# Kernel optimization log

Measured on AMD Instinct MI355X. Metric: run time of the kernel, lower is better.

The kernel has to match this reference:

```python
import jax, jax.numpy as jnp
import numpy as np

NEG_BIG = -1.0e9


def setup_inputs() -> dict:
    key = jax.random.key(0)
    ks = jax.random.split(key, 6)
    B, H, L, D = 2, 16, 2048, 64
    q = jax.random.normal(ks[0], (B, H, L, D), dtype=jnp.float32)
    k = jax.random.normal(ks[1], (B, H, L, D), dtype=jnp.float32)
    v = jax.random.normal(ks[2], (B, H, L, D), dtype=jnp.float32)
    p_q = jax.random.normal(ks[3], (B, L, 3), dtype=jnp.float32)
    p_k = jax.random.normal(ks[4], (B, L, 3), dtype=jnp.float32)
    mask = jax.random.randint(ks[5], (B, L), 0, 2, dtype=jnp.int32)
    return {"q": q, "k": k, "v": v, "p_q": p_q, "p_k": p_k, "mask": mask}


def reference(q, k, v, p_q, p_k, mask):
    # learned score function instantiated as scaled dot-product: [B,H,Lq,Lk]
    d_head = q.shape[-1]
    scores = jnp.einsum("bhqd,bhkd->bhqk", q, k) / jnp.sqrt(jnp.float32(d_head))
    # mask: [B, Lk] -> [B, 1, 1, Lk]; additive -1e9 on masked keys
    m = mask.astype(scores.dtype)[:, None, None, :]
    scores = scores + m * NEG_BIG
    # softplus normalization (instead of softmax), scaled by key length v.shape[2]
    Lk = v.shape[2]
    scores = jax.nn.softplus(scores) / Lk
    out = jnp.einsum("bhqk,bhkd->bhqd", scores, v)
    return (out, scores)
```

## Files before the change

kernel.cpp:

```cpp
#include <hip/hip_runtime.h>

typedef float f32x4  __attribute__((ext_vector_type(4)));
typedef float f32x16 __attribute__((ext_vector_type(16)));
typedef short s16x8  __attribute__((ext_vector_type(8)));
typedef unsigned int u32;
typedef unsigned int u32x4 __attribute__((ext_vector_type(4)));
typedef unsigned short u16;

#define LL 2048
#define DD 64
#define NITER 32
#define SC_OFF 4194304ull

struct SMem {
    u16 Khi[2][64][72];
    u16 VT [2][64][72];
    unsigned char P[4][4096];
};

__device__ __forceinline__ u32 cvt_pk_bf16(float lo, float hi) {
    u32 r;
    asm("v_cvt_pk_bf16_f32 %0, %1, %2" : "=v"(r) : "v"(lo), "v"(hi));
    return r;
}

__global__ __launch_bounds__(512, 4)
void psam_kernel(const float* __restrict__ Qg0, const float* __restrict__ Kg0,
                 const float* __restrict__ Vg0, const int* __restrict__ Mg0,
                 float* __restrict__ out)
{
    __shared__ SMem sm;
    const int tid = threadIdx.x;
    const int w = tid >> 6, l = tid & 63;
    const int j31 = l & 31, h = l >> 5;
    const int cw = w & 1, iw = w >> 1;
    const int cwj = cw * 32 + j31;

    const int bid = ((int)blockIdx.x & 7) * 64 + ((int)blockIdx.x >> 3);
    const int bh = bid >> 4;
    const int m0 = (bid & 15) << 7;
    const int bB = bh >> 4;

    const float* Kg = Kg0 + (size_t)bh * LL * DD;
    const float* Vg = Vg0 + (size_t)bh * LL * DD;
    const int*   Mg = Mg0 + (size_t)bB * LL;
    float* So = out + SC_OFF + (size_t)bh * LL * LL + (size_t)m0 * LL;
    float* Oo = out + ((size_t)bh * LL + m0) * DD;

    s16x8 qf[4];
    {
        const float* qr = Qg0 + ((size_t)bh * LL + m0 + iw * 32 + j31) * DD + h * 8;
#pragma unroll
        for (int ks = 0; ks < 4; ++ks) {
            f32x4 a = *(const f32x4*)(qr + ks * 16);
            f32x4 b = *(const f32x4*)(qr + ks * 16 + 4);
            u32x4 qp;
            qp[0] = cvt_pk_bf16(a[0], a[1]);
            qp[1] = cvt_pk_bf16(a[2], a[3]);
            qp[2] = cvt_pk_bf16(b[0], b[1]);
            qp[3] = cvt_pk_bf16(b[2], b[3]);
            qf[ks] = __builtin_bit_cast(s16x8, qp);
        }
    }

    const int kc = tid >> 3, kd = (tid & 7) * 8;
    const int vc = tid & 63, vd = (tid >> 6) * 8;
    f32x4 kvx, kvy, vvx, vvy;
    {
        const f32x4* s = (const f32x4*)(Kg + (size_t)kc * DD + kd);
        f32x4 x = s[0], y = s[1];
        u32x4 kp;
        kp[0] = cvt_pk_bf16(x[0], x[1]);
        kp[1] = cvt_pk_bf16(x[2], x[3]);
        kp[2] = cvt_pk_bf16(y[0], y[1]);
        kp[3] = cvt_pk_bf16(y[2], y[3]);
        *(u32x4*)&sm.Khi[0][kc][kd] = kp;
        const f32x4* s2 = (const f32x4*)(Vg + (size_t)vc * DD + vd);
        f32x4 vx = s2[0], vy = s2[1];
#pragma unroll
        for (int i = 0; i < 2; ++i) {
            u32 a0 = cvt_pk_bf16(vx[2 * i], vx[2 * i + 1]);
            sm.VT[0][vd + 2 * i][vc]     = (u16)a0;
            sm.VT[0][vd + 2 * i + 1][vc] = (u16)(a0 >> 16);
            u32 a1 = cvt_pk_bf16(vy[2 * i], vy[2 * i + 1]);
            sm.VT[0][vd + 4 + 2 * i][vc]     = (u16)a1;
            sm.VT[0][vd + 4 + 2 * i + 1][vc] = (u16)(a1 >> 16);
        }
    }
    {
        const f32x4* s = (const f32x4*)(Kg + (size_t)(64 + kc) * DD + kd);
        kvx = s[0]; kvy = s[1];
        const f32x4* s2 = (const f32x4*)(Vg + (size_t)(64 + vc) * DD + vd);
        vvx = s2[0]; vvy = s2[1];
    }
    float blc = -1.0e9f * (float)Mg[cwj];
    float bln = -1.0e9f * (float)Mg[64 + cwj];

    f32x16 accO;
#pragma unroll
    for (int e = 0; e < 16; ++e) accO[e] = 0.0f;

    unsigned char* spw = &sm.P[iw][0];
    asm volatile("s_waitcnt lgkmcnt(0)" ::: "memory");
    __builtin_amdgcn_s_barrier();

    f32x16 pA;
#pragma unroll
    for (int e = 0; e < 16; ++e) pA[e] = 0.0f;
    float* spA = So;

    int buf = 0;
    for (int t = 0; t < NITER; ++t) {
        f32x16 accS;
#pragma unroll
        for (int e = 0; e < 16; ++e) accS[e] = 0.0f;
#pragma unroll
        for (int ks = 0; ks < 4; ++ks) {
            s16x8 kf = *(const s16x8*)&sm.Khi[buf][cwj][ks * 16 + h * 8];
            accS = __builtin_amdgcn_mfma_f32_32x32x16_bf16(qf[ks], kf, accS, 0, 0, 0);
        }
        const float bl = blc;
        float* sp = So + (size_t)(iw * 32 + 4 * h) * LL + t * 64 + cwj;
        f32x16 pc;
#pragma unroll
        for (int g = 0; g < 4; ++g) {
#pragma unroll
            for (int r = 0; r < 4; ++r) {
                float x  = accS[g * 4 + r] * 0.125f + bl;
                float tt = __builtin_amdgcn_exp2f(x * 1.44269504f);
                float p  = __builtin_amdgcn_logf(1.0f + tt) * 3.38450771757785852e-4f;
                pc[g * 4 + r] = p;
                const int il = 8 * g + 4 * h + r;
                *(u16*)(spw + ((il * 128 + cwj * 2) ^ ((il & 7) << 4))) = (u16)cvt_pk_bf16(p, p);
            }
        }
        if ((t & 1) == 0) {
            pA = pc; spA = sp;
        } else {
#pragma unroll
            for (int g = 0; g < 4; ++g)
#pragma unroll
                for (int r = 0; r < 4; ++r) {
                    float* ra = spA + (size_t)(8 * g + r) * LL;
                    __builtin_nontemporal_store(pA[g * 4 + r], ra);
                    __builtin_nontemporal_store(pc[g * 4 + r], ra + 64);
                }
        }
        asm volatile("s_waitcnt lgkmcnt(0)" ::: "memory");
        __builtin_amdgcn_s_barrier();

#pragma unroll
        for (int ks = 0; ks < 4; ++ks) {
            s16x8 va = *(const s16x8*)&sm.VT[buf][cwj][ks * 16 + h * 8];
            s16x8 pb = *(const s16x8*)(spw + ((j31 * 128 + ks * 32 + h * 16) ^ ((j31 & 7) << 4)));
            accO = __builtin_amdgcn_mfma_f32_32x32x16_bf16(va, pb, accO, 0, 0, 0);
        }

        if (t + 1 < NITER) {
            u32x4 kp;
            kp[0] = cvt_pk_bf16(kvx[0], kvx[1]);
            kp[1] = cvt_pk_bf16(kvx[2], kvx[3]);
            kp[2] = cvt_pk_bf16(kvy[0], kvy[1]);
            kp[3] = cvt_pk_bf16(kvy[2], kvy[3]);
            *(u32x4*)&sm.Khi[buf ^ 1][kc][kd] = kp;
#pragma unroll
            for (int i = 0; i < 2; ++i) {
                u32 a0 = cvt_pk_bf16(vvx[2 * i], vvx[2 * i + 1]);
                sm.VT[buf ^ 1][vd + 2 * i][vc]     = (u16)a0;
                sm.VT[buf ^ 1][vd + 2 * i + 1][vc] = (u16)(a0 >> 16);
                u32 a1 = cvt_pk_bf16(vvy[2 * i], vvy[2 * i + 1]);
                sm.VT[buf ^ 1][vd + 4 + 2 * i][vc]     = (u16)a1;
                sm.VT[buf ^ 1][vd + 4 + 2 * i + 1][vc] = (u16)(a1 >> 16);
            }
        }
        {
            const int tp = (t + 2 < NITER) ? (t + 2) : (NITER - 1);
            const f32x4* s1 = (const f32x4*)(Kg + (size_t)(tp * 64 + kc) * DD + kd);
            kvx = s1[0]; kvy = s1[1];
            const f32x4* s2 = (const f32x4*)(Vg + (size_t)(tp * 64 + vc) * DD + vd);
            vvx = s2[0]; vvy = s2[1];
            blc = bln;
            bln = -1.0e9f * (float)Mg[tp * 64 + cwj];
        }
        asm volatile("s_waitcnt lgkmcnt(0)" ::: "memory");
        __builtin_amdgcn_s_barrier();
        buf ^= 1;
    }

#pragma unroll
    for (int g = 0; g < 4; ++g) {
        f32x4 o;
#pragma unroll
        for (int r = 0; r < 4; ++r) o[r] = accO[g * 4 + r];
        *(f32x4*)(Oo + (size_t)(iw * 32 + j31) * DD + cw * 32 + h * 4 + g * 8) = o;
    }
}

extern "C" void kernel_launch(void* const* d_in, const int* in_sizes, int n_in,
                              void* d_out, int out_size, void* d_ws, size_t ws_size,
                              hipStream_t stream) {
    const float* q    = (const float*)d_in[0];
    const float* k    = (const float*)d_in[1];
    const float* v    = (const float*)d_in[2];
    const int*   mask = (const int*)d_in[5];
    float* out = (float*)d_out;
    hipLaunchKernelGGL(psam_kernel, dim3(512), dim3(512), 0, stream, q, k, v, mask, out);
}
```

Baseline: 122.3 us.

## Make P tile wave-private and split PV by key half to drop a barrier

Each wave now writes its own 32x32 bf16 probability tile into a private LDS slot and multiplies it against both halves of V^T over only its own 32 keys. That removes the cross-wave dependency on P, so the workgroup barrier between the score and PV phases is dropped. Each wave therefore produces a partial O covering all 64 head dimensions, and the partial O values from the two key-half waves are summed through LDS once after the loop. The cost is a second accumulator (more VGPRs) and an extra LDS reduction plus barrier at the end.

```diff
diff --git a/kernel.cpp b/kernel.cpp
--- a/kernel.cpp
+++ b/kernel.cpp
@@ -15,7 +15,7 @@
 struct SMem {
     u16 Khi[2][64][72];
     u16 VT [2][64][72];
-    unsigned char P[4][4096];
+    u16 P[8][32][40];
 };
 
 __device__ __forceinline__ u32 cvt_pk_bf16(float lo, float hi) {
@@ -96,11 +96,11 @@
     float blc = -1.0e9f * (float)Mg[cwj];
     float bln = -1.0e9f * (float)Mg[64 + cwj];
 
-    f32x16 accO;
-#pragma unroll
-    for (int e = 0; e < 16; ++e) accO[e] = 0.0f;
-
-    unsigned char* spw = &sm.P[iw][0];
+    f32x16 accO0, accO1;
+#pragma unroll
+    for (int e = 0; e < 16; ++e) { accO0[e] = 0.0f; accO1[e] = 0.0f; }
+
+    u16* spw = &sm.P[w][0][0];
     asm volatile("s_waitcnt lgkmcnt(0)" ::: "memory");
     __builtin_amdgcn_s_barrier();
 
@@ -131,7 +131,7 @@
                 float p  = __builtin_amdgcn_logf(1.0f + tt) * 3.38450771757785852e-4f;
                 pc[g * 4 + r] = p;
                 const int il = 8 * g + 4 * h + r;
-                *(u16*)(spw + ((il * 128 + cwj * 2) ^ ((il & 7) << 4))) = (u16)cvt_pk_bf16(p, p);
+                spw[il * 40 + j31] = (u16)cvt_pk_bf16(p, p);
             }
         }
         if ((t & 1) == 0) {
@@ -147,13 +147,14 @@
                 }
         }
         asm volatile("s_waitcnt lgkmcnt(0)" ::: "memory");
-        __builtin_amdgcn_s_barrier();
-
-#pragma unroll
-        for (int ks = 0; ks < 4; ++ks) {
-            s16x8 va = *(const s16x8*)&sm.VT[buf][cwj][ks * 16 + h * 8];
-            s16x8 pb = *(const s16x8*)(spw + ((j31 * 128 + ks * 32 + h * 16) ^ ((j31 & 7) << 4)));
-            accO = __builtin_amdgcn_mfma_f32_32x32x16_bf16(va, pb, accO, 0, 0, 0);
+
+#pragma unroll
+        for (int ks2 = 0; ks2 < 2; ++ks2) {
+            s16x8 pb = *(const s16x8*)(spw + j31 * 40 + ks2 * 16 + h * 8);
+            s16x8 va0 = *(const s16x8*)&sm.VT[buf][j31][cw * 32 + ks2 * 16 + h * 8];
+            accO0 = __builtin_amdgcn_mfma_f32_32x32x16_bf16(va0, pb, accO0, 0, 0, 0);
+            s16x8 va1 = *(const s16x8*)&sm.VT[buf][32 + j31][cw * 32 + ks2 * 16 + h * 8];
+            accO1 = __builtin_amdgcn_mfma_f32_32x32x16_bf16(va1, pb, accO1, 0, 0, 0);
         }
 
         if (t + 1 < NITER) {
@@ -187,12 +188,38 @@
         buf ^= 1;
     }
 
-#pragma unroll
-    for (int g = 0; g < 4; ++g) {
-        f32x4 o;
-#pragma unroll
-        for (int r = 0; r < 4; ++r) o[r] = accO[g * 4 + r];
-        *(f32x4*)(Oo + (size_t)(iw * 32 + j31) * DD + cw * 32 + h * 4 + g * 8) = o;
+    float* red = (float*)&sm;
+    if (cw == 1) {
+#pragma unroll
+        for (int db = 0; db < 2; ++db) {
+            const f32x16& a = db ? accO1 : accO0;
+#pragma unroll
+            for (int g = 0; g < 4; ++g)
+#pragma unroll
+                for (int r = 0; r < 4; ++r) {
+                    const int row = db * 32 + 8 * g + 4 * h + r;
+                    red[(size_t)(iw * 64 + row) * 32 + j31] = a[g * 4 + r];
+                }
+        }
+    }
+    asm volatile("s_waitcnt lgkmcnt(0)" ::: "memory");
+    __builtin_amdgcn_s_barrier();
+    if (cw == 0) {
+        float* op = Oo + (size_t)(iw * 32 + j31) * DD;
+#pragma unroll
+        for (int db = 0; db < 2; ++db) {
+            const f32x16& a = db ? accO1 : accO0;
+#pragma unroll
+            for (int g = 0; g < 4; ++g) {
+                f32x4 o;
+#pragma unroll
+                for (int r = 0; r < 4; ++r) {
+                    const int row = db * 32 + 8 * g + 4 * h + r;
+                    o[r] = a[g * 4 + r] + red[(size_t)(iw * 64 + row) * 32 + j31];
+                }
+                *(f32x4*)(op + db * 32 + 8 * g + 4 * h) = o;
+            }
+        }
     }
 }
 
```

After: 121.4 us (median of 2 runs). About the same (-0.7%).

## Give each wave full 64-key strips and double the query tile per block

Applied to the files above, without the earlier changes.

Each block now covers 256 query rows, with each of the 8 waves owning 32 rows and all 64 keys per step, so the grid shrinks from 512 to 256 blocks. Every K/V tile loaded into LDS is now reused across twice as many queries. Each wave keeps its own padded P buffer, which removes the barrier between the softplus write and the PV MFMA. Score stores are batched across four iterations to write 256-float contiguous runs. The cost is higher register pressure (launch bounds lowered to 2 blocks per SM, six extra 16-float accumulators) and fewer blocks to spread across the CUs.

```diff
diff --git a/kernel.cpp b/kernel.cpp
--- a/kernel.cpp
+++ b/kernel.cpp
@@ -15,7 +15,7 @@
 struct SMem {
     u16 Khi[2][64][72];
     u16 VT [2][64][72];
-    unsigned char P[4][4096];
+    u16 P  [8][32][72];
 };
 
 __device__ __forceinline__ u32 cvt_pk_bf16(float lo, float hi) {
@@ -24,7 +24,7 @@
     return r;
 }
 
-__global__ __launch_bounds__(512, 4)
+__global__ __launch_bounds__(512, 2)
 void psam_kernel(const float* __restrict__ Qg0, const float* __restrict__ Kg0,
                  const float* __restrict__ Vg0, const int* __restrict__ Mg0,
                  float* __restrict__ out)
@@ -33,12 +33,10 @@
     const int tid = threadIdx.x;
     const int w = tid >> 6, l = tid & 63;
     const int j31 = l & 31, h = l >> 5;
-    const int cw = w & 1, iw = w >> 1;
-    const int cwj = cw * 32 + j31;
-
-    const int bid = ((int)blockIdx.x & 7) * 64 + ((int)blockIdx.x >> 3);
-    const int bh = bid >> 4;
-    const int m0 = (bid & 15) << 7;
+
+    const int bid = ((int)blockIdx.x & 7) * 32 + ((int)blockIdx.x >> 3);
+    const int bh = bid >> 3;
+    const int m0 = (bid & 7) << 8;
     const int bB = bh >> 4;
 
     const float* Kg = Kg0 + (size_t)bh * LL * DD;
@@ -49,7 +47,7 @@
 
     s16x8 qf[4];
     {
-        const float* qr = Qg0 + ((size_t)bh * LL + m0 + iw * 32 + j31) * DD + h * 8;
+        const float* qr = Qg0 + ((size_t)bh * LL + m0 + w * 32 + j31) * DD + h * 8;
 #pragma unroll
         for (int ks = 0; ks < 4; ++ks) {
             f32x4 a = *(const f32x4*)(qr + ks * 16);
@@ -93,106 +91,131 @@
         const f32x4* s2 = (const f32x4*)(Vg + (size_t)(64 + vc) * DD + vd);
         vvx = s2[0]; vvy = s2[1];
     }
-    float blc = -1.0e9f * (float)Mg[cwj];
-    float bln = -1.0e9f * (float)Mg[64 + cwj];
-
-    f32x16 accO;
-#pragma unroll
-    for (int e = 0; e < 16; ++e) accO[e] = 0.0f;
-
-    unsigned char* spw = &sm.P[iw][0];
+    float blo = -1.0e9f * (float)Mg[j31];
+    float bhi = -1.0e9f * (float)Mg[32 + j31];
+    float nlo = -1.0e9f * (float)Mg[64 + j31];
+    float nhi = -1.0e9f * (float)Mg[96 + j31];
+
+    f32x16 accO0, accO1;
+#pragma unroll
+    for (int e = 0; e < 16; ++e) { accO0[e] = 0.0f; accO1[e] = 0.0f; }
+
+    u16* spw = &sm.P[w][0][0];
     asm volatile("s_waitcnt lgkmcnt(0)" ::: "memory");
     __builtin_amdgcn_s_barrier();
 
-    f32x16 pA;
-#pragma unroll
-    for (int e = 0; e < 16; ++e) pA[e] = 0.0f;
-    float* spA = So;
-
-    int buf = 0;
-    for (int t = 0; t < NITER; ++t) {
-        f32x16 accS;
-#pragma unroll
-        for (int e = 0; e < 16; ++e) accS[e] = 0.0f;
-#pragma unroll
-        for (int ks = 0; ks < 4; ++ks) {
-            s16x8 kf = *(const s16x8*)&sm.Khi[buf][cwj][ks * 16 + h * 8];
-            accS = __builtin_amdgcn_mfma_f32_32x32x16_bf16(qf[ks], kf, accS, 0, 0, 0);
-        }
-        const float bl = blc;
-        float* sp = So + (size_t)(iw * 32 + 4 * h) * LL + t * 64 + cwj;
-        f32x16 pc;
+    f32x16 dAlo, dAhi, dBlo, dBhi, dClo, dChi;
+
+    for (int t4 = 0; t4 < NITER / 4; ++t4) {
+#pragma unroll
+        for (int p = 0; p < 4; ++p) {
+            const int t = t4 * 4 + p;
+            const int buf = p & 1;
+
+            f32x16 aS0, aS1;
+#pragma unroll
+            for (int e = 0; e < 16; ++e) { aS0[e] = 0.0f; aS1[e] = 0.0f; }
+#pragma unroll
+            for (int ks = 0; ks < 4; ++ks) {
+                s16x8 kf0 = *(const s16x8*)&sm.Khi[buf][j31][ks * 16 + h * 8];
+                aS0 = __builtin_amdgcn_mfma_f32_32x32x16_bf16(qf[ks], kf0, aS0, 0, 0, 0);
+                s16x8 kf1 = *(const s16x8*)&sm.Khi[buf][32 + j31][ks * 16 + h * 8];
+                aS1 = __builtin_amdgcn_mfma_f32_32x32x16_bf16(qf[ks], kf1, aS1, 0, 0, 0);
+            }
+
+            f32x16 plo, phi;
+#pragma unroll
+            for (int g = 0; g < 4; ++g) {
+#pragma unroll
+                for (int r = 0; r < 4; ++r) {
+                    const int e = g * 4 + r;
+                    float x0  = aS0[e] * 0.125f + blo;
+                    float t0  = __builtin_amdgcn_exp2f(x0 * 1.44269504f);
+                    plo[e] = __builtin_amdgcn_logf(1.0f + t0) * 3.38450771757785852e-4f;
+                    float x1  = aS1[e] * 0.125f + bhi;
+                    float t1  = __builtin_amdgcn_exp2f(x1 * 1.44269504f);
+                    phi[e] = __builtin_amdgcn_logf(1.0f + t1) * 3.38450771757785852e-4f;
+                    const int il = 8 * g + 4 * h + r;
+                    spw[il * 72 + j31]      = (u16)cvt_pk_bf16(plo[e], plo[e]);
+                    spw[il * 72 + 32 + j31] = (u16)cvt_pk_bf16(phi[e], phi[e]);
+                }
+            }
+
+            if (p == 0)      { dAlo = plo; dAhi = phi; }
+            else if (p == 1) { dBlo = plo; dBhi = phi; }
+            else if (p == 2) { dClo = plo; dChi = phi; }
+            else {
+                float* base = So + (size_t)(w * 32 + 4 * h) * LL + (size_t)(t4 * 4) * 64 + j31;
+#pragma unroll
+                for (int g = 0; g < 4; ++g)
+#pragma unroll
+                    for (int r = 0; r < 4; ++r) {
+                        const int e = g * 4 + r;
+                        float* ra = base + (size_t)(8 * g + r) * LL;
+                        __builtin_nontemporal_store(dAlo[e], ra);
+                        __builtin_nontemporal_store(dAhi[e], ra + 32);
+                        __builtin_nontemporal_store(dBlo[e], ra + 64);
+                        __builtin_nontemporal_store(dBhi[e], ra + 96);
+                        __builtin_nontemporal_store(dClo[e], ra + 128);
+                        __builtin_nontemporal_store(dChi[e], ra + 160);
+                        __builtin_nontemporal_store(plo[e],  ra + 192);
+                        __builtin_nontemporal_store(phi[e],  ra + 224);
+                    }
+            }
+            asm volatile("s_waitcnt lgkmcnt(0)" ::: "memory");
+
+#pragma unroll
+            for (int ks2 = 0; ks2 < 4; ++ks2) {
+                s16x8 pb = *(const s16x8*)((const char*)spw + j31 * 144 + ks2 * 32 + h * 16);
+                s16x8 va0 = *(const s16x8*)&sm.VT[buf][j31][ks2 * 16 + h * 8];
+                accO0 = __builtin_amdgcn_mfma_f32_32x32x16_bf16(va0, pb, accO0, 0, 0, 0);
+                s16x8 va1 = *(const s16x8*)&sm.VT[buf][32 + j31][ks2 * 16 + h * 8];
+                accO1 = __builtin_amdgcn_mfma_f32_32x32x16_bf16(va1, pb, accO1, 0, 0, 0);
+            }
+
+            if (t + 1 < NITER) {
+                u32x4 kp;
+                kp[0] = cvt_pk_bf16(kvx[0], kvx[1]);
+                kp[1] = cvt_pk_bf16(kvx[2], kvx[3]);
+                kp[2] = cvt_pk_bf16(kvy[0], kvy[1]);
+                kp[3] = cvt_pk_bf16(kvy[2], kvy[3]);
+                *(u32x4*)&sm.Khi[buf ^ 1][kc][kd] = kp;
+#pragma unroll
+                for (int i = 0; i < 2; ++i) {
+                    u32 a0 = cvt_pk_bf16(vvx[2 * i], vvx[2 * i + 1]);
+                    sm.VT[buf ^ 1][vd + 2 * i][vc]     = (u16)a0;
+                    sm.VT[buf ^ 1][vd + 2 * i + 1][vc] = (u16)(a0 >> 16);
+                    u32 a1 = cvt_pk_bf16(vvy[2 * i], vvy[2 * i + 1]);
+                    sm.VT[buf ^ 1][vd + 4 + 2 * i][vc]     = (u16)a1;
+                    sm.VT[buf ^ 1][vd + 4 + 2 * i + 1][vc] = (u16)(a1 >> 16);
+                }
+            }
+            {
+                const int tp = (t + 2 < NITER) ? (t + 2) : (NITER - 1);
+                const f32x4* s1 = (const f32x4*)(Kg + (size_t)(tp * 64 + kc) * DD + kd);
+                kvx = s1[0]; kvy = s1[1];
+                const f32x4* s2 = (const f32x4*)(Vg + (size_t)(tp * 64 + vc) * DD + vd);
+                vvx = s2[0]; vvy = s2[1];
+                blo = nlo; bhi = nhi;
+                nlo = -1.0e9f * (float)Mg[tp * 64 + j31];
+                nhi = -1.0e9f * (float)Mg[tp * 64 + 32 + j31];
+            }
+            asm volatile("s_waitcnt lgkmcnt(0)" ::: "memory");
+            __builtin_amdgcn_s_barrier();
+        }
+    }
+
+    float* op = Oo + (size_t)(w * 32 + j31) * DD;
+#pragma unroll
+    for (int db = 0; db < 2; ++db) {
+        const f32x16& a = db ? accO1 : accO0;
 #pragma unroll
         for (int g = 0; g < 4; ++g) {
-#pragma unroll
-            for (int r = 0; r < 4; ++r) {
-                float x  = accS[g * 4 + r] * 0.125f + bl;
-                float tt = __builtin_amdgcn_exp2f(x * 1.44269504f);
-                float p  = __builtin_amdgcn_logf(1.0f + tt) * 3.38450771757785852e-4f;
-                pc[g * 4 + r] = p;
-                const int il = 8 * g + 4 * h + r;
-                *(u16*)(spw + ((il * 128 + cwj * 2) ^ ((il & 7) << 4))) = (u16)cvt_pk_bf16(p, p);
-            }
-        }
-        if ((t & 1) == 0) {
-            pA = pc; spA = sp;
-        } else {
-#pragma unroll
-            for (int g = 0; g < 4; ++g)
-#pragma unroll
-                for (int r = 0; r < 4; ++r) {
-                    float* ra = spA + (size_t)(8 * g + r) * LL;
-                    __builtin_nontemporal_store(pA[g * 4 + r], ra);
-                    __builtin_nontemporal_store(pc[g * 4 + r], ra + 64);
-                }
-        }
-        asm volatile("s_waitcnt lgkmcnt(0)" ::: "memory");
-        __builtin_amdgcn_s_barrier();
-
-#pragma unroll
-        for (int ks = 0; ks < 4; ++ks) {
-            s16x8 va = *(const s16x8*)&sm.VT[buf][cwj][ks * 16 + h * 8];
-            s16x8 pb = *(const s16x8*)(spw + ((j31 * 128 + ks * 32 + h * 16) ^ ((j31 & 7) << 4)));
-            accO = __builtin_amdgcn_mfma_f32_32x32x16_bf16(va, pb, accO, 0, 0, 0);
-        }
-
-        if (t + 1 < NITER) {
-            u32x4 kp;
-            kp[0] = cvt_pk_bf16(kvx[0], kvx[1]);
-            kp[1] = cvt_pk_bf16(kvx[2], kvx[3]);
-            kp[2] = cvt_pk_bf16(kvy[0], kvy[1]);
-            kp[3] = cvt_pk_bf16(kvy[2], kvy[3]);
-            *(u32x4*)&sm.Khi[buf ^ 1][kc][kd] = kp;
-#pragma unroll
-            for (int i = 0; i < 2; ++i) {
-                u32 a0 = cvt_pk_bf16(vvx[2 * i], vvx[2 * i + 1]);
-                sm.VT[buf ^ 1][vd + 2 * i][vc]     = (u16)a0;
-                sm.VT[buf ^ 1][vd + 2 * i + 1][vc] = (u16)(a0 >> 16);
-                u32 a1 = cvt_pk_bf16(vvy[2 * i], vvy[2 * i + 1]);
-                sm.VT[buf ^ 1][vd + 4 + 2 * i][vc]     = (u16)a1;
-                sm.VT[buf ^ 1][vd + 4 + 2 * i + 1][vc] = (u16)(a1 >> 16);
-            }
-        }
-        {
-            const int tp = (t + 2 < NITER) ? (t + 2) : (NITER - 1);
-            const f32x4* s1 = (const f32x4*)(Kg + (size_t)(tp * 64 + kc) * DD + kd);
-            kvx = s1[0]; kvy = s1[1];
-            const f32x4* s2 = (const f32x4*)(Vg + (size_t)(tp * 64 + vc) * DD + vd);
-            vvx = s2[0]; vvy = s2[1];
-            blc = bln;
-            bln = -1.0e9f * (float)Mg[tp * 64 + cwj];
-        }
-        asm volatile("s_waitcnt lgkmcnt(0)" ::: "memory");
-        __builtin_amdgcn_s_barrier();
-        buf ^= 1;
-    }
-
-#pragma unroll
-    for (int g = 0; g < 4; ++g) {
-        f32x4 o;
-#pragma unroll
-        for (int r = 0; r < 4; ++r) o[r] = accO[g * 4 + r];
-        *(f32x4*)(Oo + (size_t)(iw * 32 + j31) * DD + cw * 32 + h * 4 + g * 8) = o;
+            f32x4 o;
+#pragma unroll
+            for (int r = 0; r < 4; ++r) o[r] = a[g * 4 + r];
+            *(f32x4*)(op + db * 32 + 8 * g + 4 * h) = o;
+        }
     }
 }
 
@@ -204,5 +227,5 @@
     const float* v    = (const float*)d_in[2];
     const int*   mask = (const int*)d_in[5];
     float* out = (float*)d_out;
-    hipLaunchKernelGGL(psam_kernel, dim3(512), dim3(512), 0, stream, q, k, v, mask, out);
+    hipLaunchKernelGGL(psam_kernel, dim3(256), dim3(512), 0, stream, q, k, v, mask, out);
 }
```

After: 141.1 us. 1.15x slower.
